# Performance work log

Measured on AMD Instinct MI355X. Metric: run time of the kernel, lower is better.

## Reference

```python
import jax, jax.numpy as jnp
import numpy as np

N_HEAD = 12
SEQ = 4096
D_MODEL = 768


def setup_inputs() -> dict:
    key = jax.random.key(0)
    ks = jax.random.split(key, 5)
    tokens = jax.random.normal(ks[0], (SEQ, D_MODEL), dtype=jnp.float32)
    # GPT-2 causal mask buffer: lower-triangular ones, shape [1,1,n_ctx,n_ctx]
    attn_bias = jnp.tril(jnp.ones((SEQ, SEQ), dtype=jnp.float32))[None, None]
    c_attn_weight = jax.random.normal(ks[1], (D_MODEL, 3 * D_MODEL), dtype=jnp.float32) * 0.02
    c_attn_bias = jax.random.normal(ks[2], (3 * D_MODEL,), dtype=jnp.float32) * 0.02
    c_proj_weight = jax.random.normal(ks[3], (D_MODEL, D_MODEL), dtype=jnp.float32) * 0.02
    c_proj_bias = jax.random.normal(ks[4], (D_MODEL,), dtype=jnp.float32) * 0.02
    return {
        "tokens": tokens,
        "attn_bias": attn_bias,
        "c_attn_weight": c_attn_weight,
        "c_attn_bias": c_attn_bias,
        "c_proj_weight": c_proj_weight,
        "c_proj_bias": c_proj_bias,
    }


def reference(tokens, attn_bias, c_attn_weight, c_attn_bias, c_proj_weight, c_proj_bias):
    S, D = tokens.shape
    H = N_HEAD
    hd = D // H
    qkv = tokens @ c_attn_weight + c_attn_bias          # [S, 3D]
    q, k, v = jnp.split(qkv, 3, axis=1)                 # each [S, D]
    q = q.reshape(S, H, hd).transpose(1, 0, 2)          # [H, S, hd]
    kh = k.reshape(S, H, hd).transpose(1, 2, 0)         # [H, hd, S] (key pre-transposed)
    vh = v.reshape(S, H, hd).transpose(1, 0, 2)         # [H, S, hd]
    w = jnp.einsum('hqd,hdk->hqk', q, kh) / jnp.sqrt(jnp.float32(hd))  # [H, S, S]
    nd, ns = S, S
    b = attn_bias[0, :, ns - nd:ns, :ns]                # [1, S, S], broadcasts over heads
    w = w * b - 1e10 * (1.0 - b)
    p = jax.nn.softmax(w, axis=-1)
    a = jnp.einsum('hqk,hkd->hqd', p, vh)               # [H, S, hd]
    a = a.transpose(1, 0, 2).reshape(S, D)              # merge heads
    out = a @ c_proj_weight + c_proj_bias               # [S, D]
    return out
```

## Files before the change

### kernel.cpp

```cpp
#include <hip/hip_runtime.h>

typedef __attribute__((ext_vector_type(8))) short s8v;
typedef __attribute__((ext_vector_type(2))) float f32x2;
typedef __attribute__((ext_vector_type(4))) float f32x4;
typedef __attribute__((ext_vector_type(16))) float f32x16;
typedef __attribute__((ext_vector_type(4))) unsigned short u16x4;
typedef __attribute__((ext_vector_type(4))) unsigned int u32x4;
typedef __attribute__((ext_vector_type(4))) _Float16 h16x4;

#define SEQ 4096
#define DM  768
#define NH  12
#define HD  64
#define QSCL 0.18033688f
#define FOFF 8.0f

__device__ __forceinline__ unsigned short f2bf(float f) {
  union { float f; unsigned int u; } v; v.f = f;
  unsigned int r = v.u + 0x7fffu + ((v.u >> 16) & 1u);
  return (unsigned short)(r >> 16);
}

__device__ __forceinline__ unsigned int cvtpk(float lo, float hi) {
  unsigned int r;
  asm("v_cvt_pk_bf16_f32 %0, %1, %2" : "=v"(r) : "v"(lo), "v"(hi));
  return r;
}

__device__ __forceinline__ void gload16(const void* g, void* l) {
  __builtin_amdgcn_global_load_lds((const __attribute__((address_space(1))) void*)g,
                                   (__attribute__((address_space(3))) void*)l, 16, 0, 0);
}

__global__ __launch_bounds__(256) void k_prep(
    const float* __restrict__ tokens, const float* __restrict__ wqkv,
    const float* __restrict__ wproj, unsigned short* __restrict__ tok,
    unsigned short* __restrict__ wqkvT, unsigned short* __restrict__ wprojT) {
  __shared__ float tile[32][33];
  const int b = blockIdx.x;
  const int tid = threadIdx.x;
  if (b < 3072) {
    int i = (b * 256 + tid) * 4;
    float4 v = *reinterpret_cast<const float4*>(tokens + i);
    u16x4 o;
    o.x = f2bf(v.x); o.y = f2bf(v.y); o.z = f2bf(v.z); o.w = f2bf(v.w);
    *reinterpret_cast<u16x4*>(tok + i) = o;
    return;
  }
  const float* in;
  unsigned short* out;
  int idx, N;
  if (b < 4800) { idx = b - 3072; in = wqkv;  out = wqkvT;  N = 2304; }
  else          { idx = b - 4800; in = wproj; out = wprojT; N = 768;  }
  const int k0 = (idx % 24) * 32, n0 = (idx / 24) * 32;
  const int tr = tid >> 5, tc = tid & 31;
#pragma unroll
  for (int i = 0; i < 4; i++)
    tile[i * 8 + tr][tc] = in[(k0 + i * 8 + tr) * N + n0 + tc];
  __syncthreads();
#pragma unroll
  for (int i = 0; i < 4; i++)
    out[(n0 + i * 8 + tr) * 768 + k0 + tc] = f2bf(tile[tc][i * 8 + tr]);
}

template<int MODE>
__global__ __launch_bounds__(256) void k_gemm(
    const unsigned short* __restrict__ A, const unsigned short* __restrict__ BT,
    const float* __restrict__ bias,
    unsigned short* __restrict__ Oq, unsigned short* __restrict__ Ok,
    unsigned short* __restrict__ Ov, float* __restrict__ Of) {
  __shared__ unsigned short As[128 * 32];
  __shared__ unsigned short Bs[128 * 32];
  const int tid = threadIdx.x;
  const int lane = tid & 63;
  const int w = tid >> 6;
  const int wm = w >> 1, wn = w & 1;
  const int l15 = lane & 15, l4 = lane >> 4;
  const int m0 = blockIdx.x * 128, n0 = blockIdx.y * 128;

  f32x4 acc[4][4] = {};

  int srow[2], skc[2];
#pragma unroll
  for (int j = 0; j < 2; j++) {
    int slot = j * 256 + tid;
    srow[j] = slot >> 2;
    skc[j] = (slot & 3) ^ ((srow[j] >> 1) & 3);
  }
  const int ldsb0 = (tid & ~63) * 16;
  const int ldsb1 = (256 + (tid & ~63)) * 16;

  for (int k0 = 0; k0 < DM; k0 += 32) {
    gload16(A + (m0 + srow[0]) * DM + k0 + skc[0] * 8, (char*)As + ldsb0);
    gload16(A + (m0 + srow[1]) * DM + k0 + skc[1] * 8, (char*)As + ldsb1);
    gload16(BT + (n0 + srow[0]) * DM + k0 + skc[0] * 8, (char*)Bs + ldsb0);
    gload16(BT + (n0 + srow[1]) * DM + k0 + skc[1] * 8, (char*)Bs + ldsb1);
    __syncthreads();
    s8v af[4], bfr[4];
#pragma unroll
    for (int i = 0; i < 4; i++) {
      int ra = wm * 64 + i * 16 + l15;
      int ca = (l4 ^ ((ra >> 1) & 3)) * 8;
      af[i] = *reinterpret_cast<const s8v*>(&As[ra * 32 + ca]);
      int rb = wn * 64 + i * 16 + l15;
      int cb = (l4 ^ ((rb >> 1) & 3)) * 8;
      bfr[i] = *reinterpret_cast<const s8v*>(&Bs[rb * 32 + cb]);
    }
#pragma unroll
    for (int mi = 0; mi < 4; mi++)
#pragma unroll
      for (int nj = 0; nj < 4; nj++)
        acc[mi][nj] = __builtin_amdgcn_mfma_f32_16x16x32_bf16(af[mi], bfr[nj], acc[mi][nj], 0, 0, 0);
    __syncthreads();
  }

#pragma unroll
  for (int nj = 0; nj < 4; nj++) {
    const int col = n0 + wn * 64 + nj * 16 + l15;
    const float bv = bias[col];
#pragma unroll
    for (int mi = 0; mi < 4; mi++) {
      const int rowb = m0 + wm * 64 + mi * 16 + l4 * 4;
      if (MODE == 0) {
        if (col < 768) {
#pragma unroll
          for (int r = 0; r < 4; r++)
            Oq[(rowb + r) * DM + col] = f2bf((acc[mi][nj][r] + bv) * QSCL);
        } else if (col < 1536) {
#pragma unroll
          for (int r = 0; r < 4; r++)
            Ok[(rowb + r) * DM + (col - 768)] = f2bf(acc[mi][nj][r] + bv);
        } else {
          u16x4 pk;
#pragma unroll
          for (int r = 0; r < 4; r++)
            pk[r] = f2bf(acc[mi][nj][r] + bv);
          *reinterpret_cast<u16x4*>(&Ov[(col - 1536) * SEQ + rowb]) = pk;
        }
      } else {
#pragma unroll
        for (int r = 0; r < 4; r++)
          Of[(rowb + r) * DM + col] = acc[mi][nj][r] + bv;
      }
    }
  }
}

__global__ __launch_bounds__(256, 4) void k_attn(
    const unsigned short* __restrict__ Qb, const unsigned short* __restrict__ Kb,
    const unsigned short* __restrict__ Vt, _Float16* __restrict__ Opart,
    float* __restrict__ lw) {
  __shared__ unsigned short Ks[2][64 * 64];
  __shared__ unsigned short Vs[2][64 * 64];
  const int tid = threadIdx.x;
  const int lane = tid & 63;
  const int w = tid >> 6;
  const int l31 = lane & 31, lh = lane >> 5;
  const int bid = blockIdx.x;
  const int s = bid & 3;
  const int b2 = bid >> 2;
  const int head = b2 % NH;
  const int pi = b2 / NH;

  const unsigned short* const Kh = Kb + head * HD;
  const unsigned short* const Vh = Vt + head * HD * SEQ;

  int srow[2], scol[2];
#pragma unroll
  for (int j = 0; j < 2; j++) {
    int c = j * 256 + tid;
    srow[j] = c >> 3;
    scol[j] = ((c & 7) ^ (srow[j] & 7)) * 8;
  }
  const int ldsoff0 = (tid & ~63) * 16;
  const int ldsoff1 = 4096 + (tid & ~63) * 16;
  const int x7 = l31 & 7;
  const int rbase = l31 * 128;

#pragma unroll 1
  for (int half = 0; half < 2; half++) {
    const int qt = half ? pi : 31 - pi;
    const int q0w = qt * 128 + w * 32;
    const int ntiles = 2 * qt + 2;

    int koff0 = (s * 64 + srow[0]) * DM + scol[0];
    int koff1 = (s * 64 + srow[1]) * DM + scol[1];
    int voff0 = srow[0] * SEQ + s * 64 + scol[0];
    int voff1 = srow[1] * SEQ + s * 64 + scol[1];

    s8v aq[4];
#pragma unroll
    for (int kc = 0; kc < 4; kc++)
      aq[kc] = *reinterpret_cast<const s8v*>(
          &Qb[(q0w + l31) * DM + head * HD + kc * 16 + lh * 8]);

    f32x16 O0 = {}, O1 = {};
    float lsum = 0.f;

    if (s < ntiles) {
      gload16(Kh + koff0, (char*)Ks[0] + ldsoff0);
      gload16(Kh + koff1, (char*)Ks[0] + ldsoff1);
      gload16(Vh + voff0, (char*)Vs[0] + ldsoff0);
      gload16(Vh + voff1, (char*)Vs[0] + ldsoff1);
      __asm__ volatile("s_waitcnt vmcnt(0)" ::: "memory");
    }
    __syncthreads();
    koff0 += 256 * DM; koff1 += 256 * DM;
    voff0 += 256;      voff1 += 256;

    for (int t = s; t < ntiles; t += 4) {
      const int cur = ((t - s) >> 2) & 1;
      if (t + 4 < ntiles) {
        const int nxt = cur ^ 1;
        gload16(Kh + koff0, (char*)Ks[nxt] + ldsoff0);
        gload16(Kh + koff1, (char*)Ks[nxt] + ldsoff1);
        gload16(Vh + voff0, (char*)Vs[nxt] + ldsoff0);
        gload16(Vh + voff1, (char*)Vs[nxt] + ldsoff1);
      }
      koff0 += 256 * DM; koff1 += 256 * DM;
      voff0 += 256;      voff1 += 256;
      const int kb = t * 64;
      if (kb <= q0w + 31) {
        const char* const kbuf = (const char*)Ks[cur];
        const char* const vbuf = (const char*)Vs[cur];
        f32x16 z0, z1;
#pragma unroll
        for (int r = 0; r < 16; r++) { z0[r] = -FOFF; z1[r] = -FOFF; }
        __builtin_amdgcn_s_setprio(1);
#pragma unroll
        for (int kc = 0; kc < 4; kc++) {
          const int so = ((kc * 2 + lh) ^ x7) << 4;
          const s8v k0 = *reinterpret_cast<const s8v*>(kbuf + rbase + so);
          const s8v k1 = *reinterpret_cast<const s8v*>(kbuf + 4096 + rbase + so);
          z0 = __builtin_amdgcn_mfma_f32_32x32x16_bf16(k0, aq[kc], z0, 0, 0, 0);
          z1 = __builtin_amdgcn_mfma_f32_32x32x16_bf16(k1, aq[kc], z1, 0, 0, 0);
        }
        __builtin_amdgcn_s_setprio(0);
        if (kb + 63 > q0w) {
          const int qm = q0w + l31 - kb - 4 * lh;
#pragma unroll
          for (int r = 0; r < 16; r++) {
            const int koff = (r & 3) + 8 * (r >> 2);
            z0[r] = (koff > qm) ? -1e30f : z0[r];
            z1[r] = (koff + 32 > qm) ? -1e30f : z1[r];
          }
        }
        f32x2 sa = {0.f, 0.f}, sb = {0.f, 0.f};
#pragma unroll
        for (int r = 0; r < 8; r++) {
          z0[2 * r] = exp2f(z0[2 * r]);
          z0[2 * r + 1] = exp2f(z0[2 * r + 1]);
          f32x2 e0; e0[0] = z0[2 * r]; e0[1] = z0[2 * r + 1];
          sa += e0;
          z1[2 * r] = exp2f(z1[2 * r]);
          z1[2 * r + 1] = exp2f(z1[2 * r + 1]);
          f32x2 e1; e1[0] = z1[2 * r]; e1[1] = z1[2 * r + 1];
          sb += e1;
        }
        sa += sb;
        lsum += sa[0] + sa[1];
        s8v pf[4];
#define PACKKC(V, base, dst)                                                 \
        {                                                                    \
          unsigned int A0 = cvtpk(V[base + 0], V[base + 1]);                 \
          unsigned int B0 = cvtpk(V[base + 2], V[base + 3]);                 \
          unsigned int A1 = cvtpk(V[base + 4], V[base + 5]);                 \
          unsigned int B1 = cvtpk(V[base + 6], V[base + 7]);                 \
          asm("v_permlane32_swap_b32 %0, %1" : "+v"(A0), "+v"(A1));          \
          asm("v_permlane32_swap_b32 %0, %1" : "+v"(B0), "+v"(B1));          \
          u32x4 q_ = {A0, B0, A1, B1};                                       \
          dst = __builtin_bit_cast(s8v, q_);                                 \
        }
        PACKKC(z0, 0, pf[0]);
        PACKKC(z0, 8, pf[1]);
        PACKKC(z1, 0, pf[2]);
        PACKKC(z1, 8, pf[3]);
#undef PACKKC
        __builtin_amdgcn_s_setprio(1);
#pragma unroll
        for (int kc = 0; kc < 4; kc++) {
          const int so = ((kc * 2 + lh) ^ x7) << 4;
          const s8v v0 = *reinterpret_cast<const s8v*>(vbuf + rbase + so);
          const s8v v1 = *reinterpret_cast<const s8v*>(vbuf + 4096 + rbase + so);
          O0 = __builtin_amdgcn_mfma_f32_32x32x16_bf16(v0, pf[kc], O0, 0, 0, 0);
          O1 = __builtin_amdgcn_mfma_f32_32x32x16_bf16(v1, pf[kc], O1, 0, 0, 0);
        }
        __builtin_amdgcn_s_setprio(0);
      }
      __asm__ volatile("s_waitcnt vmcnt(0)" ::: "memory");
      __syncthreads();
    }

    lsum += __shfl_xor(lsum, 32);
    _Float16* const op = Opart + (size_t)s * SEQ * DM + (size_t)(q0w + l31) * DM +
                         head * HD + 4 * lh;
#pragma unroll
    for (int k = 0; k < 4; k++) {
      h16x4 o0h, o1h;
#pragma unroll
      for (int r = 0; r < 4; r++) {
        o0h[r] = (_Float16)O0[k * 4 + r];
        o1h[r] = (_Float16)O1[k * 4 + r];
      }
      *reinterpret_cast<h16x4*>(op + 8 * k) = o0h;
      *reinterpret_cast<h16x4*>(op + 32 + 8 * k) = o1h;
    }
    if (lh == 0)
      lw[(s * NH + head) * SEQ + q0w + l31] = lsum;
    __syncthreads();
  }
}

__global__ __launch_bounds__(256) void k_merge(const _Float16* __restrict__ Opart,
                                               const float* __restrict__ lw,
                                               unsigned short* __restrict__ attn) {
  const int idx = blockIdx.x * 256 + threadIdx.x;
  const int e4 = idx * 4;
  const int row = e4 / DM;
  const int col = e4 - row * DM;
  const int head = col >> 6;
  const float l0 = lw[(0 * NH + head) * SEQ + row];
  const float l1 = lw[(1 * NH + head) * SEQ + row];
  const float l2 = lw[(2 * NH + head) * SEQ + row];
  const float l3 = lw[(3 * NH + head) * SEQ + row];
  const float rl = 1.f / (l0 + l1 + l2 + l3);
  const size_t SD = (size_t)SEQ * DM;
  const h16x4 o0 = *reinterpret_cast<const h16x4*>(Opart + e4);
  const h16x4 o1 = *reinterpret_cast<const h16x4*>(Opart + SD + e4);
  const h16x4 o2 = *reinterpret_cast<const h16x4*>(Opart + 2 * SD + e4);
  const h16x4 o3 = *reinterpret_cast<const h16x4*>(Opart + 3 * SD + e4);
  u16x4 pk;
#pragma unroll
  for (int j = 0; j < 4; j++)
    pk[j] = f2bf(((float)o0[j] + (float)o1[j] + (float)o2[j] + (float)o3[j]) * rl);
  *reinterpret_cast<u16x4*>(attn + e4) = pk;
}

extern "C" void kernel_launch(void* const* d_in, const int* in_sizes, int n_in,
                              void* d_out, int out_size, void* d_ws, size_t ws_size,
                              hipStream_t stream) {
  (void)in_sizes; (void)n_in; (void)out_size; (void)ws_size;
  const float* tokens = (const float*)d_in[0];
  const float* wqkv  = (const float*)d_in[2];
  const float* bqkv  = (const float*)d_in[3];
  const float* wproj = (const float*)d_in[4];
  const float* bproj = (const float*)d_in[5];
  float* out = (float*)d_out;

  unsigned short* tok    = (unsigned short*)d_ws;
  unsigned short* wqkvT  = tok + 4096 * 768;
  unsigned short* wprojT = wqkvT + 2304 * 768;
  unsigned short* Qb     = wprojT + 768 * 768;
  unsigned short* Kb     = Qb + 4096 * 768;
  unsigned short* Vt     = Kb + 4096 * 768;
  unsigned short* attn   = Vt + 768 * 4096;
  _Float16* Opart = (_Float16*)(attn + 4096 * 768);
  float* lw = (float*)(Opart + 4 * (size_t)4096 * 768);

  k_prep<<<5376, 256, 0, stream>>>(tokens, wqkv, wproj, tok, wqkvT, wprojT);
  k_gemm<0><<<dim3(32, 18), 256, 0, stream>>>(tok, wqkvT, bqkv, Qb, Kb, Vt, nullptr);
  k_attn<<<768, 256, 0, stream>>>(Qb, Kb, Vt, Opart, lw);
  k_merge<<<3072, 256, 0, stream>>>(Opart, lw, attn);
  k_gemm<1><<<dim3(32, 6), 256, 0, stream>>>(attn, wprojT, bproj, nullptr, nullptr, nullptr, out);
}
```

Before: 112.0 us.

## Schedule attention work units dynamically with atomic counter and 8-way KV split

Replaces the static per-block assignment of causal attention tiles with a persistent-style loop that fetches work units through a global atomic counter, ordering units longest first. Query tiles in the upper half of the sequence now split their KV range eight ways instead of four, and the merge kernel sums eight partials for those rows. The goal is better load balance across CUs for the triangular workload. In exchange it costs a memset, a block-wide sync per unit, and more partial-output traffic, and it reuses the token buffer for the attention output.

```diff
diff --git a/kernel.cpp b/kernel.cpp
--- a/kernel.cpp
+++ b/kernel.cpp
@@ -14,6 +14,7 @@
 #define HD  64
 #define QSCL 0.18033688f
 #define FOFF 8.0f
+#define NUNITS 2304
 
 __device__ __forceinline__ unsigned short f2bf(float f) {
   union { float f; unsigned int u; } v; v.f = f;
@@ -149,21 +150,14 @@
 __global__ __launch_bounds__(256, 4) void k_attn(
     const unsigned short* __restrict__ Qb, const unsigned short* __restrict__ Kb,
     const unsigned short* __restrict__ Vt, _Float16* __restrict__ Opart,
-    float* __restrict__ lw) {
+    float* __restrict__ lw, int* __restrict__ ctr) {
   __shared__ unsigned short Ks[2][64 * 64];
   __shared__ unsigned short Vs[2][64 * 64];
+  __shared__ int su;
   const int tid = threadIdx.x;
   const int lane = tid & 63;
   const int w = tid >> 6;
   const int l31 = lane & 31, lh = lane >> 5;
-  const int bid = blockIdx.x;
-  const int s = bid & 3;
-  const int b2 = bid >> 2;
-  const int head = b2 % NH;
-  const int pi = b2 / NH;
-
-  const unsigned short* const Kh = Kb + head * HD;
-  const unsigned short* const Vh = Vt + head * HD * SEQ;
 
   int srow[2], scol[2];
 #pragma unroll
@@ -177,11 +171,33 @@
   const int x7 = l31 & 7;
   const int rbase = l31 * 128;
 
-#pragma unroll 1
-  for (int half = 0; half < 2; half++) {
-    const int qt = half ? pi : 31 - pi;
+  while (true) {
+    if (tid == 0) su = atomicAdd(ctr, 1);
+    __syncthreads();
+    const int u = su;
+    if (u >= NUNITS) break;
+
+    int qt, head, s, nsplit;
+    if (u < 1536) {
+      qt = 31 - u / 96;
+      const int r = u % 96;
+      head = r >> 3;
+      s = r & 7;
+      nsplit = 8;
+    } else {
+      const int v = u - 1536;
+      qt = 15 - v / 48;
+      const int r = v % 48;
+      head = r >> 2;
+      s = r & 3;
+      nsplit = 4;
+    }
     const int q0w = qt * 128 + w * 32;
     const int ntiles = 2 * qt + 2;
+    const unsigned short* const Kh = Kb + head * HD;
+    const unsigned short* const Vh = Vt + head * HD * SEQ;
+    const int kstep = nsplit * 64 * DM;
+    const int vstep = nsplit * 64;
 
     int koff0 = (s * 64 + srow[0]) * DM + scol[0];
     int koff1 = (s * 64 + srow[1]) * DM + scol[1];
@@ -205,20 +221,20 @@
       __asm__ volatile("s_waitcnt vmcnt(0)" ::: "memory");
     }
     __syncthreads();
-    koff0 += 256 * DM; koff1 += 256 * DM;
-    voff0 += 256;      voff1 += 256;
-
-    for (int t = s; t < ntiles; t += 4) {
-      const int cur = ((t - s) >> 2) & 1;
-      if (t + 4 < ntiles) {
+    koff0 += kstep; koff1 += kstep;
+    voff0 += vstep; voff1 += vstep;
+
+    int cur = 0;
+    for (int t = s; t < ntiles; t += nsplit) {
+      if (t + nsplit < ntiles) {
         const int nxt = cur ^ 1;
         gload16(Kh + koff0, (char*)Ks[nxt] + ldsoff0);
         gload16(Kh + koff1, (char*)Ks[nxt] + ldsoff1);
         gload16(Vh + voff0, (char*)Vs[nxt] + ldsoff0);
         gload16(Vh + voff1, (char*)Vs[nxt] + ldsoff1);
       }
-      koff0 += 256 * DM; koff1 += 256 * DM;
-      voff0 += 256;      voff1 += 256;
+      koff0 += kstep; koff1 += kstep;
+      voff0 += vstep; voff1 += vstep;
       const int kb = t * 64;
       if (kb <= q0w + 31) {
         const char* const kbuf = (const char*)Ks[cur];
@@ -289,6 +305,7 @@
       }
       __asm__ volatile("s_waitcnt vmcnt(0)" ::: "memory");
       __syncthreads();
+      cur ^= 1;
     }
 
     lsum += __shfl_xor(lsum, 32);
@@ -319,20 +336,29 @@
   const int row = e4 / DM;
   const int col = e4 - row * DM;
   const int head = col >> 6;
-  const float l0 = lw[(0 * NH + head) * SEQ + row];
-  const float l1 = lw[(1 * NH + head) * SEQ + row];
-  const float l2 = lw[(2 * NH + head) * SEQ + row];
-  const float l3 = lw[(3 * NH + head) * SEQ + row];
-  const float rl = 1.f / (l0 + l1 + l2 + l3);
   const size_t SD = (size_t)SEQ * DM;
-  const h16x4 o0 = *reinterpret_cast<const h16x4*>(Opart + e4);
-  const h16x4 o1 = *reinterpret_cast<const h16x4*>(Opart + SD + e4);
-  const h16x4 o2 = *reinterpret_cast<const h16x4*>(Opart + 2 * SD + e4);
-  const h16x4 o3 = *reinterpret_cast<const h16x4*>(Opart + 3 * SD + e4);
+  float l = 0.f;
+  float acc[4] = {0.f, 0.f, 0.f, 0.f};
+#pragma unroll
+  for (int s = 0; s < 4; s++) {
+    l += lw[(s * NH + head) * SEQ + row];
+    const h16x4 o = *reinterpret_cast<const h16x4*>(Opart + s * SD + e4);
+#pragma unroll
+    for (int j = 0; j < 4; j++) acc[j] += (float)o[j];
+  }
+  if (row >= 2048) {
+#pragma unroll
+    for (int s = 4; s < 8; s++) {
+      l += lw[(s * NH + head) * SEQ + row];
+      const h16x4 o = *reinterpret_cast<const h16x4*>(Opart + s * SD + e4);
+#pragma unroll
+      for (int j = 0; j < 4; j++) acc[j] += (float)o[j];
+    }
+  }
+  const float rl = 1.f / l;
   u16x4 pk;
 #pragma unroll
-  for (int j = 0; j < 4; j++)
-    pk[j] = f2bf(((float)o0[j] + (float)o1[j] + (float)o2[j] + (float)o3[j]) * rl);
+  for (int j = 0; j < 4; j++) pk[j] = f2bf(acc[j] * rl);
   *reinterpret_cast<u16x4*>(attn + e4) = pk;
 }
 
@@ -353,13 +379,15 @@
   unsigned short* Qb     = wprojT + 768 * 768;
   unsigned short* Kb     = Qb + 4096 * 768;
   unsigned short* Vt     = Kb + 4096 * 768;
-  unsigned short* attn   = Vt + 768 * 4096;
-  _Float16* Opart = (_Float16*)(attn + 4096 * 768);
-  float* lw = (float*)(Opart + 4 * (size_t)4096 * 768);
-
+  _Float16* Opart = (_Float16*)(Vt + 768 * 4096);
+  float* lw = (float*)(Opart + 8 * (size_t)4096 * 768);
+  int* ctr = (int*)(lw + 8 * NH * SEQ);
+  unsigned short* attn = tok;
+
+  hipMemsetAsync(ctr, 0, sizeof(int), stream);
   k_prep<<<5376, 256, 0, stream>>>(tokens, wqkv, wproj, tok, wqkvT, wprojT);
   k_gemm<0><<<dim3(32, 18), 256, 0, stream>>>(tok, wqkvT, bqkv, Qb, Kb, Vt, nullptr);
-  k_attn<<<768, 256, 0, stream>>>(Qb, Kb, Vt, Opart, lw);
+  k_attn<<<1280, 256, 0, stream>>>(Qb, Kb, Vt, Opart, lw, ctr);
   k_merge<<<3072, 256, 0, stream>>>(Opart, lw, attn);
   k_gemm<1><<<dim3(32, 6), 256, 0, stream>>>(attn, wprojT, bproj, nullptr, nullptr, nullptr, out);
 }
```

After: 132.7 us. 1.18x slower.
